# Optimization experiments

Hardware: AMD Instinct MI355X
Metric: run time of the kernel (lower is better)

## Reference

```python
import jax, jax.numpy as jnp
import numpy as np

SCALE = 0.08838834764831845  # 1/sqrt(128)


def setup_inputs() -> dict:
    key = jax.random.key(0)
    k1, k2, k3, k4 = jax.random.split(key, 4)
    B, Sq, H, D = 1, 2048, 32, 128
    Skv, K = 4096, 256
    return {
        "q": jax.random.normal(k1, (B, Sq, H, D), jnp.float32),
        "kv": jax.random.normal(k2, (B, Skv, 2, D), jnp.float32),  # stacked K,V (MQA)
        "attn_sink": jax.random.normal(k3, (H,), jnp.float32),
        "topk_idxs": jax.random.randint(k4, (B, Sq, K), 0, Skv),
    }


def reference(q, kv, attn_sink, topk_idxs):
    # q:        [B, Sq, H, D]
    # kv:       [B, Skv, 2, D]  (index 0 = keys, 1 = values; shared across heads)
    # topk_idxs:[B, Sq, K]      per-query selected KV positions
    # attn_sink:[H]             per-head sink logit added to the softmax denominator
    B = q.shape[0]
    # Gather selected KV per query: [B, Sq, K, 2, D]
    gathered = kv[jnp.arange(B)[:, None, None], topk_idxs]
    k = gathered[..., 0, :]  # [B, Sq, K, D]
    v = gathered[..., 1, :]  # [B, Sq, K, D]

    scores = jnp.einsum("bqhd,bqkd->bqhk", q, k) * SCALE  # [B, Sq, H, K]
    sink = attn_sink[None, None, :, None]                  # [1, 1, H, 1]

    # Numerically stable softmax over K selected tokens + sink logit.
    m = jnp.maximum(jnp.max(scores, axis=-1, keepdims=True), sink)
    e = jnp.exp(scores - m)
    denom = jnp.sum(e, axis=-1, keepdims=True) + jnp.exp(sink - m)
    probs = e / denom                                      # sink absorbs leftover mass

    out = jnp.einsum("bqhk,bqkd->bqhd", probs, v)          # [B, Sq, H, D]
    return out
```

## Files before the change

### kernel.cpp

```cpp
#include <hip/hip_runtime.h>
#include <hip/hip_bf16.h>

#define SQ 2048
#define NH 32
#define DH 128
#define NK 256
#define SCALE 0.08838834764831845f

typedef __attribute__((ext_vector_type(8))) __bf16 bf16x8;
typedef __attribute__((ext_vector_type(4))) float floatx4;
typedef __attribute__((ext_vector_type(4))) unsigned short ushort4_t;

#define QS_STRIDE 136
#define KS_STRIDE 136
#define VB_STRIDE 72
#define PB_STRIDE 264

#define OFF_KV   16896
#define OFF_TOPK 35328
#define OFF_SINK 36352
#define OFF_RED  36480
#define OFF_RED2 36992
#define SMEM_SZ  37504

__device__ __forceinline__ unsigned short f2bf(float x) {
  union { float f; unsigned int u; } v; v.f = x;
  unsigned int r = v.u + 0x7FFFu + ((v.u >> 16) & 1u);
  return (unsigned short)(r >> 16);
}

template <int CTRL>
__device__ __forceinline__ float dpp_rot(float x) {
  int i = __builtin_bit_cast(int, x);
  i = __builtin_amdgcn_mov_dpp(i, CTRL, 0xF, 0xF, true);
  return __builtin_bit_cast(float, i);
}
#define RED16_MAX(v) { v = fmaxf(v, dpp_rot<0x121>(v)); v = fmaxf(v, dpp_rot<0x122>(v)); \
                       v = fmaxf(v, dpp_rot<0x124>(v)); v = fmaxf(v, dpp_rot<0x128>(v)); }
#define RED16_SUM(v) { v += dpp_rot<0x121>(v); v += dpp_rot<0x122>(v); \
                       v += dpp_rot<0x124>(v); v += dpp_rot<0x128>(v); }

__global__ __launch_bounds__(256) void kv_to_bf16(const float* __restrict__ kv,
                                                  unsigned short* __restrict__ kvb) {
  int i = blockIdx.x * 256 + threadIdx.x;
  float4 f = ((const float4*)kv)[i];
  ushort4_t u = { f2bf(f.x), f2bf(f.y), f2bf(f.z), f2bf(f.w) };
  ((ushort4_t*)kvb)[i] = u;
}

__global__ __launch_bounds__(256, 4) void sparse_attn_kernel(
    const float* __restrict__ q, const unsigned short* __restrict__ kvb,
    const float* __restrict__ sink, const int* __restrict__ topk,
    float* __restrict__ out) {
  __shared__ __align__(16) char smem[SMEM_SZ];
  unsigned short* qs    = (unsigned short*)smem;
  unsigned short* pbuf  = (unsigned short*)smem;
  unsigned short* kvbuf = (unsigned short*)(smem + OFF_KV);
  int*   topk_s = (int*)(smem + OFF_TOPK);
  float* sink_s = (float*)(smem + OFF_SINK);
  float* red    = (float*)(smem + OFF_RED);
  float* red2   = (float*)(smem + OFF_RED2);

  const int tid = threadIdx.x;
  const int s = blockIdx.x;
  const int wave = tid >> 6;
  const int lane = tid & 63;
  const int quad = lane >> 4;
  const int l16 = lane & 15;

  topk_s[tid] = topk[(size_t)s * NK + tid];
  if (tid < 32) sink_s[tid] = sink[tid];
  {
    int r = tid >> 2, seg = tid & 3;
    int idx = topk[(size_t)s * NK + r];
    const unsigned short* kp = kvb + (size_t)idx * 256 + seg * 32;
    unsigned short* dst = &kvbuf[r * KS_STRIDE + seg * 32];
#pragma unroll
    for (int i = 0; i < 4; i++)
      *(uint4*)&dst[i * 8] = *(const uint4*)&kp[i * 8];
  }
  {
    const float* qp = q + (size_t)s * (NH * DH);
    int h = tid >> 3;
    int d0 = (tid & 7) * 16;
#pragma unroll
    for (int i = 0; i < 4; i++) {
      float4 f = *(const float4*)(qp + h * DH + d0 + i * 4);
      ushort4_t u = { f2bf(f.x * SCALE), f2bf(f.y * SCALE),
                      f2bf(f.z * SCALE), f2bf(f.w * SCALE) };
      *(ushort4_t*)&qs[h * QS_STRIDE + d0 + i * 4] = u;
    }
  }
  __syncthreads();

  bf16x8 afrag[2][4];
#pragma unroll
  for (int mt = 0; mt < 2; mt++)
#pragma unroll
    for (int ks = 0; ks < 4; ks++)
      afrag[mt][ks] =
          *(const bf16x8*)&qs[(mt * 16 + l16) * QS_STRIDE + ks * 32 + quad * 8];

  floatx4 sc[4][2];
#pragma unroll 1
  for (int c = 0; c < 4; c++) {
    floatx4 a0 = {0.f, 0.f, 0.f, 0.f};
    floatx4 a1 = {0.f, 0.f, 0.f, 0.f};
    const int nrow = wave * 16 + l16;
#pragma unroll
    for (int ks = 0; ks < 4; ks++) {
      bf16x8 b = *(const bf16x8*)&kvbuf[nrow * KS_STRIDE + ks * 32 + quad * 8];
      a0 = __builtin_amdgcn_mfma_f32_16x16x32_bf16(afrag[0][ks], b, a0, 0, 0, 0);
      a1 = __builtin_amdgcn_mfma_f32_16x16x32_bf16(afrag[1][ks], b, a1, 0, 0, 0);
    }
    sc[c][0] = a0;
    sc[c][1] = a1;
    __syncthreads();
    if (c < 3) {
      int r = tid >> 2, seg = tid & 3;
      int idx = topk_s[(c + 1) * 64 + r];
      const unsigned short* kp = kvb + (size_t)idx * 256 + seg * 32;
      unsigned short* dst = &kvbuf[r * KS_STRIDE + seg * 32];
#pragma unroll
      for (int i = 0; i < 4; i++)
        *(uint4*)&dst[i * 8] = *(const uint4*)&kp[i * 8];
      __syncthreads();
    }
  }

  {
    int rg = tid & 15, dg = tid >> 4;
    int r0 = rg * 4, d0 = dg * 8;
    int4 idx4 = *(const int4*)&topk_s[r0];
    uint4 ra = *(const uint4*)(kvb + (size_t)idx4.x * 256 + 128 + d0);
    uint4 rb = *(const uint4*)(kvb + (size_t)idx4.y * 256 + 128 + d0);
    uint4 rc = *(const uint4*)(kvb + (size_t)idx4.z * 256 + 128 + d0);
    uint4 rd = *(const uint4*)(kvb + (size_t)idx4.w * 256 + 128 + d0);
    const unsigned* pa = (const unsigned*)&ra;
    const unsigned* pb = (const unsigned*)&rb;
    const unsigned* pc = (const unsigned*)&rc;
    const unsigned* pd = (const unsigned*)&rd;
#pragma unroll
    for (int w = 0; w < 4; w++) {
      unsigned lo01 = __builtin_amdgcn_perm(pb[w], pa[w], 0x05040100u);
      unsigned lo23 = __builtin_amdgcn_perm(pd[w], pc[w], 0x05040100u);
      unsigned hi01 = __builtin_amdgcn_perm(pb[w], pa[w], 0x07060302u);
      unsigned hi23 = __builtin_amdgcn_perm(pd[w], pc[w], 0x07060302u);
      uint2 lo = { lo01, lo23 }, hi = { hi01, hi23 };
      *(uint2*)&kvbuf[(d0 + 2 * w) * VB_STRIDE + r0] = lo;
      *(uint2*)&kvbuf[(d0 + 2 * w + 1) * VB_STRIDE + r0] = hi;
    }
  }

  float mh[2][4];
#pragma unroll
  for (int mt = 0; mt < 2; mt++)
#pragma unroll
    for (int r = 0; r < 4; r++) {
      float v = fmaxf(fmaxf(sc[0][mt][r], sc[1][mt][r]),
                      fmaxf(sc[2][mt][r], sc[3][mt][r]));
      RED16_MAX(v);
      mh[mt][r] = v;
    }
  if (l16 == 0) {
#pragma unroll
    for (int mt = 0; mt < 2; mt++)
#pragma unroll
      for (int r = 0; r < 4; r++)
        red[wave * 32 + mt * 16 + quad * 4 + r] = mh[mt][r];
  }
  __syncthreads();
#pragma unroll
  for (int mt = 0; mt < 2; mt++)
#pragma unroll
    for (int r = 0; r < 4; r++) {
      int h = mt * 16 + quad * 4 + r;
      float v = sink_s[h];
#pragma unroll
      for (int w = 0; w < 4; w++) v = fmaxf(v, red[w * 32 + h]);
      mh[mt][r] = v;
    }
  float ps[2][4];
#pragma unroll
  for (int mt = 0; mt < 2; mt++)
#pragma unroll
    for (int r = 0; r < 4; r++) {
      float acc = 0.f;
#pragma unroll
      for (int c = 0; c < 4; c++) {
        float e = __expf(sc[c][mt][r] - mh[mt][r]);
        sc[c][mt][r] = e;
        acc += e;
      }
      RED16_SUM(acc);
      ps[mt][r] = acc;
    }
  if (l16 == 0) {
#pragma unroll
    for (int mt = 0; mt < 2; mt++)
#pragma unroll
      for (int r = 0; r < 4; r++)
        red2[wave * 32 + mt * 16 + quad * 4 + r] = ps[mt][r];
  }
  __syncthreads();
  float inv[2][4];
#pragma unroll
  for (int mt = 0; mt < 2; mt++)
#pragma unroll
    for (int r = 0; r < 4; r++) {
      int h = mt * 16 + quad * 4 + r;
      float dd = __expf(sink_s[h] - mh[mt][r]);
#pragma unroll
      for (int w = 0; w < 4; w++) dd += red2[w * 32 + h];
      inv[mt][r] = 1.0f / dd;
    }
#pragma unroll
  for (int c = 0; c < 4; c++)
#pragma unroll
    for (int mt = 0; mt < 2; mt++)
#pragma unroll
      for (int r = 0; r < 4; r++)
        pbuf[(mt * 16 + quad * 4 + r) * PB_STRIDE + c * 64 + wave * 16 + l16] =
            f2bf(sc[c][mt][r]);
  __syncthreads();

  floatx4 oacc[2][2];
#pragma unroll
  for (int mt = 0; mt < 2; mt++)
#pragma unroll
    for (int nt = 0; nt < 2; nt++)
      oacc[mt][nt] = (floatx4){0.f, 0.f, 0.f, 0.f};

#pragma unroll 1
  for (int c = 0; c < 4; c++) {
#pragma unroll
    for (int ks = 0; ks < 2; ks++) {
      int kof = c * 64 + ks * 32 + quad * 8;
      bf16x8 a0 = *(const bf16x8*)&pbuf[l16 * PB_STRIDE + kof];
      bf16x8 a1 = *(const bf16x8*)&pbuf[(16 + l16) * PB_STRIDE + kof];
      int kl = ks * 32 + quad * 8;
      bf16x8 b0 = *(const bf16x8*)&kvbuf[(wave * 32 + l16) * VB_STRIDE + kl];
      bf16x8 b1 = *(const bf16x8*)&kvbuf[(wave * 32 + 16 + l16) * VB_STRIDE + kl];
      oacc[0][0] = __builtin_amdgcn_mfma_f32_16x16x32_bf16(a0, b0, oacc[0][0], 0, 0, 0);
      oacc[0][1] = __builtin_amdgcn_mfma_f32_16x16x32_bf16(a0, b1, oacc[0][1], 0, 0, 0);
      oacc[1][0] = __builtin_amdgcn_mfma_f32_16x16x32_bf16(a1, b0, oacc[1][0], 0, 0, 0);
      oacc[1][1] = __builtin_amdgcn_mfma_f32_16x16x32_bf16(a1, b1, oacc[1][1], 0, 0, 0);
    }
    if (c < 3) {
      __syncthreads();
      int rg = tid & 15, dg = tid >> 4;
      int r0 = rg * 4, d0 = dg * 8;
      int4 idx4 = *(const int4*)&topk_s[(c + 1) * 64 + r0];
      uint4 ra = *(const uint4*)(kvb + (size_t)idx4.x * 256 + 128 + d0);
      uint4 rb = *(const uint4*)(kvb + (size_t)idx4.y * 256 + 128 + d0);
      uint4 rc = *(const uint4*)(kvb + (size_t)idx4.z * 256 + 128 + d0);
      uint4 rd = *(const uint4*)(kvb + (size_t)idx4.w * 256 + 128 + d0);
      const unsigned* pa = (const unsigned*)&ra;
      const unsigned* pb = (const unsigned*)&rb;
      const unsigned* pc = (const unsigned*)&rc;
      const unsigned* pd = (const unsigned*)&rd;
#pragma unroll
      for (int w = 0; w < 4; w++) {
        unsigned lo01 = __builtin_amdgcn_perm(pb[w], pa[w], 0x05040100u);
        unsigned lo23 = __builtin_amdgcn_perm(pd[w], pc[w], 0x05040100u);
        unsigned hi01 = __builtin_amdgcn_perm(pb[w], pa[w], 0x07060302u);
        unsigned hi23 = __builtin_amdgcn_perm(pd[w], pc[w], 0x07060302u);
        uint2 lo = { lo01, lo23 }, hi = { hi01, hi23 };
        *(uint2*)&kvbuf[(d0 + 2 * w) * VB_STRIDE + r0] = lo;
        *(uint2*)&kvbuf[(d0 + 2 * w + 1) * VB_STRIDE + r0] = hi;
      }
      __syncthreads();
    }
  }

  {
    float* op = out + (size_t)s * (NH * DH);
#pragma unroll
    for (int mt = 0; mt < 2; mt++)
#pragma unroll
      for (int nt = 0; nt < 2; nt++)
#pragma unroll
        for (int r4 = 0; r4 < 4; r4++) {
          int h = mt * 16 + quad * 4 + r4;
          int d = wave * 32 + nt * 16 + l16;
          op[h * DH + d] = oacc[mt][nt][r4] * inv[mt][r4];
        }
  }
}

extern "C" void kernel_launch(void* const* d_in, const int* in_sizes, int n_in,
                              void* d_out, int out_size, void* d_ws, size_t ws_size,
                              hipStream_t stream) {
  (void)in_sizes; (void)n_in; (void)out_size; (void)ws_size;
  const float* q    = (const float*)d_in[0];
  const float* kv   = (const float*)d_in[1];
  const float* sink = (const float*)d_in[2];
  const int*   topk = (const int*)d_in[3];
  float* out = (float*)d_out;
  unsigned short* kvb = (unsigned short*)d_ws;

  kv_to_bf16<<<dim3(1024), dim3(256), 0, stream>>>(kv, kvb);
  sparse_attn_kernel<<<dim3(SQ), dim3(256), 0, stream>>>(q, kvb, sink, topk, out);
}
```

Baseline: 117.5 us.

## Prefetch gathered K/V chunks into registers to overlap loads with MFMA

Restructures the K and V gather loops into a register-prefetch pipeline. The next chunk's global gather is issued before the current chunk's MFMA work, and the first V chunk is loaded during the softmax phase. This is meant to hide gather latency that was previously exposed between barriers. It also folds log2(e) into the Q scale and sink so exp2 can be used directly, and replaces manual bf16 rounding with packed conversion intrinsics, at the cost of higher register pressure.

```diff
diff --git a/kernel.cpp b/kernel.cpp
--- a/kernel.cpp
+++ b/kernel.cpp
@@ -6,10 +6,10 @@
 #define DH 128
 #define NK 256
 #define SCALE 0.08838834764831845f
+#define LOG2E 1.4426950408889634f
 
 typedef __attribute__((ext_vector_type(8))) __bf16 bf16x8;
 typedef __attribute__((ext_vector_type(4))) float floatx4;
-typedef __attribute__((ext_vector_type(4))) unsigned short ushort4_t;
 
 #define QS_STRIDE 136
 #define KS_STRIDE 136
@@ -23,10 +23,18 @@
 #define OFF_RED2 36992
 #define SMEM_SZ  37504
 
-__device__ __forceinline__ unsigned short f2bf(float x) {
-  union { float f; unsigned int u; } v; v.f = x;
-  unsigned int r = v.u + 0x7FFFu + ((v.u >> 16) & 1u);
-  return (unsigned short)(r >> 16);
+__device__ __forceinline__ unsigned pk_bf16(float a, float b) {
+  union { __hip_bfloat162 h2; unsigned u; } c;
+  c.h2 = __float22bfloat162_rn(make_float2(a, b));
+  return c.u;
+}
+
+__device__ __forceinline__ float fast_exp2(float x) {
+#if __has_builtin(__builtin_amdgcn_exp2f)
+  return __builtin_amdgcn_exp2f(x);
+#else
+  return exp2f(x);
+#endif
 }
 
 template <int CTRL>
@@ -44,8 +52,93 @@
                                                   unsigned short* __restrict__ kvb) {
   int i = blockIdx.x * 256 + threadIdx.x;
   float4 f = ((const float4*)kv)[i];
-  ushort4_t u = { f2bf(f.x), f2bf(f.y), f2bf(f.z), f2bf(f.w) };
-  ((ushort4_t*)kvb)[i] = u;
+  uint2 o = { pk_bf16(f.x, f.y), pk_bf16(f.z, f.w) };
+  ((uint2*)kvb)[i] = o;
+}
+
+struct KR { uint4 v[4]; };
+struct VR { uint4 a, b, c, d; };
+
+__device__ __forceinline__ KR k_load(const unsigned short* __restrict__ kvb,
+                                     const int* __restrict__ tks, int c, int tid) {
+  int r = tid >> 2, seg = tid & 3;
+  int idx = tks[c * 64 + r];
+  const uint4* p = (const uint4*)(kvb + (size_t)idx * 256 + seg * 32);
+  KR k;
+#pragma unroll
+  for (int i = 0; i < 4; i++) k.v[i] = p[i];
+  return k;
+}
+
+__device__ __forceinline__ void k_write(unsigned short* kvbuf, const KR& k, int tid) {
+  int r = tid >> 2, seg = tid & 3;
+  uint4* d = (uint4*)&kvbuf[r * KS_STRIDE + seg * 32];
+#pragma unroll
+  for (int i = 0; i < 4; i++) d[i] = k.v[i];
+}
+
+__device__ __forceinline__ VR v_load(const unsigned short* __restrict__ kvb,
+                                     const int* tks, int c, int tid) {
+  int rg = tid & 15, dg = tid >> 4;
+  int r0 = rg * 4, d0 = dg * 8;
+  int4 i4 = *(const int4*)&tks[c * 64 + r0];
+  VR v;
+  v.a = *(const uint4*)(kvb + (size_t)i4.x * 256 + 128 + d0);
+  v.b = *(const uint4*)(kvb + (size_t)i4.y * 256 + 128 + d0);
+  v.c = *(const uint4*)(kvb + (size_t)i4.z * 256 + 128 + d0);
+  v.d = *(const uint4*)(kvb + (size_t)i4.w * 256 + 128 + d0);
+  return v;
+}
+
+__device__ __forceinline__ void v_write(unsigned short* kvbuf, const VR& v, int tid) {
+  int rg = tid & 15, dg = tid >> 4;
+  int r0 = rg * 4, d0 = dg * 8;
+  const unsigned* pa = (const unsigned*)&v.a;
+  const unsigned* pb = (const unsigned*)&v.b;
+  const unsigned* pc = (const unsigned*)&v.c;
+  const unsigned* pd = (const unsigned*)&v.d;
+#pragma unroll
+  for (int w = 0; w < 4; w++) {
+    unsigned lo01 = __builtin_amdgcn_perm(pb[w], pa[w], 0x05040100u);
+    unsigned lo23 = __builtin_amdgcn_perm(pd[w], pc[w], 0x05040100u);
+    unsigned hi01 = __builtin_amdgcn_perm(pb[w], pa[w], 0x07060302u);
+    unsigned hi23 = __builtin_amdgcn_perm(pd[w], pc[w], 0x07060302u);
+    uint2 lo = { lo01, lo23 }, hi = { hi01, hi23 };
+    *(uint2*)&kvbuf[(d0 + 2 * w) * VB_STRIDE + r0] = lo;
+    *(uint2*)&kvbuf[(d0 + 2 * w + 1) * VB_STRIDE + r0] = hi;
+  }
+}
+
+__device__ __forceinline__ void gemm1(const unsigned short* kvbuf,
+                                      const bf16x8 af[2][4], int nrow, int quad,
+                                      floatx4& a0, floatx4& a1) {
+  a0 = (floatx4){0.f, 0.f, 0.f, 0.f};
+  a1 = (floatx4){0.f, 0.f, 0.f, 0.f};
+#pragma unroll
+  for (int ks = 0; ks < 4; ks++) {
+    bf16x8 b = *(const bf16x8*)&kvbuf[nrow * KS_STRIDE + ks * 32 + quad * 8];
+    a0 = __builtin_amdgcn_mfma_f32_16x16x32_bf16(af[0][ks], b, a0, 0, 0, 0);
+    a1 = __builtin_amdgcn_mfma_f32_16x16x32_bf16(af[1][ks], b, a1, 0, 0, 0);
+  }
+}
+
+__device__ __forceinline__ void pv_chunk(const unsigned short* pbuf,
+                                         const unsigned short* kvbuf, int c,
+                                         int wave, int quad, int l16,
+                                         floatx4 oacc[2][2]) {
+#pragma unroll
+  for (int ks = 0; ks < 2; ks++) {
+    int kof = c * 64 + ks * 32 + quad * 8;
+    bf16x8 a0 = *(const bf16x8*)&pbuf[l16 * PB_STRIDE + kof];
+    bf16x8 a1 = *(const bf16x8*)&pbuf[(16 + l16) * PB_STRIDE + kof];
+    int kl = ks * 32 + quad * 8;
+    bf16x8 b0 = *(const bf16x8*)&kvbuf[(wave * 32 + l16) * VB_STRIDE + kl];
+    bf16x8 b1 = *(const bf16x8*)&kvbuf[(wave * 32 + 16 + l16) * VB_STRIDE + kl];
+    oacc[0][0] = __builtin_amdgcn_mfma_f32_16x16x32_bf16(a0, b0, oacc[0][0], 0, 0, 0);
+    oacc[0][1] = __builtin_amdgcn_mfma_f32_16x16x32_bf16(a0, b1, oacc[0][1], 0, 0, 0);
+    oacc[1][0] = __builtin_amdgcn_mfma_f32_16x16x32_bf16(a1, b0, oacc[1][0], 0, 0, 0);
+    oacc[1][1] = __builtin_amdgcn_mfma_f32_16x16x32_bf16(a1, b1, oacc[1][1], 0, 0, 0);
+  }
 }
 
 __global__ __launch_bounds__(256, 4) void sparse_attn_kernel(
@@ -67,30 +160,32 @@
   const int lane = tid & 63;
   const int quad = lane >> 4;
   const int l16 = lane & 15;
-
-  topk_s[tid] = topk[(size_t)s * NK + tid];
-  if (tid < 32) sink_s[tid] = sink[tid];
+  const int* tkg = topk + (size_t)s * NK;
+
+  topk_s[tid] = tkg[tid];
+  if (tid < 32) sink_s[tid] = sink[tid] * LOG2E;
   {
     int r = tid >> 2, seg = tid & 3;
-    int idx = topk[(size_t)s * NK + r];
-    const unsigned short* kp = kvb + (size_t)idx * 256 + seg * 32;
-    unsigned short* dst = &kvbuf[r * KS_STRIDE + seg * 32];
-#pragma unroll
-    for (int i = 0; i < 4; i++)
-      *(uint4*)&dst[i * 8] = *(const uint4*)&kp[i * 8];
+    int idx = tkg[r];
+    const uint4* p = (const uint4*)(kvb + (size_t)idx * 256 + seg * 32);
+    uint4* d = (uint4*)&kvbuf[r * KS_STRIDE + seg * 32];
+#pragma unroll
+    for (int i = 0; i < 4; i++) d[i] = p[i];
   }
   {
+    const float QSC = SCALE * LOG2E;
     const float* qp = q + (size_t)s * (NH * DH);
-    int h = tid >> 3;
-    int d0 = (tid & 7) * 16;
-#pragma unroll
-    for (int i = 0; i < 4; i++) {
-      float4 f = *(const float4*)(qp + h * DH + d0 + i * 4);
-      ushort4_t u = { f2bf(f.x * SCALE), f2bf(f.y * SCALE),
-                      f2bf(f.z * SCALE), f2bf(f.w * SCALE) };
-      *(ushort4_t*)&qs[h * QS_STRIDE + d0 + i * 4] = u;
-    }
-  }
+    int h = tid >> 3, d0 = (tid & 7) * 16;
+    const float4* src = (const float4*)(qp + h * DH + d0);
+    float4 f0 = src[0], f1 = src[1], f2 = src[2], f3 = src[3];
+    uint4 o0 = { pk_bf16(f0.x * QSC, f0.y * QSC), pk_bf16(f0.z * QSC, f0.w * QSC),
+                 pk_bf16(f1.x * QSC, f1.y * QSC), pk_bf16(f1.z * QSC, f1.w * QSC) };
+    uint4 o1 = { pk_bf16(f2.x * QSC, f2.y * QSC), pk_bf16(f2.z * QSC, f2.w * QSC),
+                 pk_bf16(f3.x * QSC, f3.y * QSC), pk_bf16(f3.z * QSC, f3.w * QSC) };
+    *(uint4*)&qs[h * QS_STRIDE + d0] = o0;
+    *(uint4*)&qs[h * QS_STRIDE + d0 + 8] = o1;
+  }
+  KR k1 = k_load(kvb, tkg, 1, tid);
   __syncthreads();
 
   bf16x8 afrag[2][4];
@@ -101,56 +196,31 @@
       afrag[mt][ks] =
           *(const bf16x8*)&qs[(mt * 16 + l16) * QS_STRIDE + ks * 32 + quad * 8];
 
+  const int nrow = wave * 16 + l16;
+
   floatx4 sc[4][2];
-#pragma unroll 1
-  for (int c = 0; c < 4; c++) {
-    floatx4 a0 = {0.f, 0.f, 0.f, 0.f};
-    floatx4 a1 = {0.f, 0.f, 0.f, 0.f};
-    const int nrow = wave * 16 + l16;
-#pragma unroll
-    for (int ks = 0; ks < 4; ks++) {
-      bf16x8 b = *(const bf16x8*)&kvbuf[nrow * KS_STRIDE + ks * 32 + quad * 8];
-      a0 = __builtin_amdgcn_mfma_f32_16x16x32_bf16(afrag[0][ks], b, a0, 0, 0, 0);
-      a1 = __builtin_amdgcn_mfma_f32_16x16x32_bf16(afrag[1][ks], b, a1, 0, 0, 0);
-    }
-    sc[c][0] = a0;
-    sc[c][1] = a1;
-    __syncthreads();
-    if (c < 3) {
-      int r = tid >> 2, seg = tid & 3;
-      int idx = topk_s[(c + 1) * 64 + r];
-      const unsigned short* kp = kvb + (size_t)idx * 256 + seg * 32;
-      unsigned short* dst = &kvbuf[r * KS_STRIDE + seg * 32];
-#pragma unroll
-      for (int i = 0; i < 4; i++)
-        *(uint4*)&dst[i * 8] = *(const uint4*)&kp[i * 8];
-      __syncthreads();
-    }
-  }
-
-  {
-    int rg = tid & 15, dg = tid >> 4;
-    int r0 = rg * 4, d0 = dg * 8;
-    int4 idx4 = *(const int4*)&topk_s[r0];
-    uint4 ra = *(const uint4*)(kvb + (size_t)idx4.x * 256 + 128 + d0);
-    uint4 rb = *(const uint4*)(kvb + (size_t)idx4.y * 256 + 128 + d0);
-    uint4 rc = *(const uint4*)(kvb + (size_t)idx4.z * 256 + 128 + d0);
-    uint4 rd = *(const uint4*)(kvb + (size_t)idx4.w * 256 + 128 + d0);
-    const unsigned* pa = (const unsigned*)&ra;
-    const unsigned* pb = (const unsigned*)&rb;
-    const unsigned* pc = (const unsigned*)&rc;
-    const unsigned* pd = (const unsigned*)&rd;
-#pragma unroll
-    for (int w = 0; w < 4; w++) {
-      unsigned lo01 = __builtin_amdgcn_perm(pb[w], pa[w], 0x05040100u);
-      unsigned lo23 = __builtin_amdgcn_perm(pd[w], pc[w], 0x05040100u);
-      unsigned hi01 = __builtin_amdgcn_perm(pb[w], pa[w], 0x07060302u);
-      unsigned hi23 = __builtin_amdgcn_perm(pd[w], pc[w], 0x07060302u);
-      uint2 lo = { lo01, lo23 }, hi = { hi01, hi23 };
-      *(uint2*)&kvbuf[(d0 + 2 * w) * VB_STRIDE + r0] = lo;
-      *(uint2*)&kvbuf[(d0 + 2 * w + 1) * VB_STRIDE + r0] = hi;
-    }
-  }
+  gemm1(kvbuf, afrag, nrow, quad, sc[0][0], sc[0][1]);
+  __syncthreads();
+  k_write(kvbuf, k1, tid);
+  KR k2 = k_load(kvb, topk_s, 2, tid);
+  __syncthreads();
+
+  gemm1(kvbuf, afrag, nrow, quad, sc[1][0], sc[1][1]);
+  __syncthreads();
+  k_write(kvbuf, k2, tid);
+  KR k3 = k_load(kvb, topk_s, 3, tid);
+  __syncthreads();
+
+  gemm1(kvbuf, afrag, nrow, quad, sc[2][0], sc[2][1]);
+  __syncthreads();
+  k_write(kvbuf, k3, tid);
+  VR v0 = v_load(kvb, topk_s, 0, tid);
+  __syncthreads();
+
+  gemm1(kvbuf, afrag, nrow, quad, sc[3][0], sc[3][1]);
+  __syncthreads();
+  v_write(kvbuf, v0, tid);
+  VR v1 = v_load(kvb, topk_s, 1, tid);
 
   float mh[2][4];
 #pragma unroll
@@ -188,7 +258,7 @@
       float acc = 0.f;
 #pragma unroll
       for (int c = 0; c < 4; c++) {
-        float e = __expf(sc[c][mt][r] - mh[mt][r]);
+        float e = fast_exp2(sc[c][mt][r] - mh[mt][r]);
         sc[c][mt][r] = e;
         acc += e;
       }
@@ -209,7 +279,7 @@
 #pragma unroll
     for (int r = 0; r < 4; r++) {
       int h = mt * 16 + quad * 4 + r;
-      float dd = __expf(sink_s[h] - mh[mt][r]);
+      float dd = fast_exp2(sink_s[h] - mh[mt][r]);
 #pragma unroll
       for (int w = 0; w < 4; w++) dd += red2[w * 32 + h];
       inv[mt][r] = 1.0f / dd;
@@ -217,11 +287,16 @@
 #pragma unroll
   for (int c = 0; c < 4; c++)
 #pragma unroll
-    for (int mt = 0; mt < 2; mt++)
-#pragma unroll
-      for (int r = 0; r < 4; r++)
-        pbuf[(mt * 16 + quad * 4 + r) * PB_STRIDE + c * 64 + wave * 16 + l16] =
-            f2bf(sc[c][mt][r]);
+    for (int mt = 0; mt < 2; mt++) {
+      int col = c * 64 + wave * 16 + l16;
+      unsigned short* pb = &pbuf[(mt * 16 + quad * 4) * PB_STRIDE + col];
+      unsigned p01 = pk_bf16(sc[c][mt][0], sc[c][mt][1]);
+      unsigned p23 = pk_bf16(sc[c][mt][2], sc[c][mt][3]);
+      pb[0] = (unsigned short)p01;
+      pb[PB_STRIDE] = (unsigned short)(p01 >> 16);
+      pb[2 * PB_STRIDE] = (unsigned short)p23;
+      pb[3 * PB_STRIDE] = (unsigned short)(p23 >> 16);
+    }
   __syncthreads();
 
   floatx4 oacc[2][2];
@@ -231,47 +306,24 @@
     for (int nt = 0; nt < 2; nt++)
       oacc[mt][nt] = (floatx4){0.f, 0.f, 0.f, 0.f};
 
-#pragma unroll 1
-  for (int c = 0; c < 4; c++) {
-#pragma unroll
-    for (int ks = 0; ks < 2; ks++) {
-      int kof = c * 64 + ks * 32 + quad * 8;
-      bf16x8 a0 = *(const bf16x8*)&pbuf[l16 * PB_STRIDE + kof];
-      bf16x8 a1 = *(const bf16x8*)&pbuf[(16 + l16) * PB_STRIDE + kof];
-      int kl = ks * 32 + quad * 8;
-      bf16x8 b0 = *(const bf16x8*)&kvbuf[(wave * 32 + l16) * VB_STRIDE + kl];
-      bf16x8 b1 = *(const bf16x8*)&kvbuf[(wave * 32 + 16 + l16) * VB_STRIDE + kl];
-      oacc[0][0] = __builtin_amdgcn_mfma_f32_16x16x32_bf16(a0, b0, oacc[0][0], 0, 0, 0);
-      oacc[0][1] = __builtin_amdgcn_mfma_f32_16x16x32_bf16(a0, b1, oacc[0][1], 0, 0, 0);
-      oacc[1][0] = __builtin_amdgcn_mfma_f32_16x16x32_bf16(a1, b0, oacc[1][0], 0, 0, 0);
-      oacc[1][1] = __builtin_amdgcn_mfma_f32_16x16x32_bf16(a1, b1, oacc[1][1], 0, 0, 0);
-    }
-    if (c < 3) {
-      __syncthreads();
-      int rg = tid & 15, dg = tid >> 4;
-      int r0 = rg * 4, d0 = dg * 8;
-      int4 idx4 = *(const int4*)&topk_s[(c + 1) * 64 + r0];
-      uint4 ra = *(const uint4*)(kvb + (size_t)idx4.x * 256 + 128 + d0);
-      uint4 rb = *(const uint4*)(kvb + (size_t)idx4.y * 256 + 128 + d0);
-      uint4 rc = *(const uint4*)(kvb + (size_t)idx4.z * 256 + 128 + d0);
-      uint4 rd = *(const uint4*)(kvb + (size_t)idx4.w * 256 + 128 + d0);
-      const unsigned* pa = (const unsigned*)&ra;
-      const unsigned* pb = (const unsigned*)&rb;
-      const unsigned* pc = (const unsigned*)&rc;
-      const unsigned* pd = (const unsigned*)&rd;
-#pragma unroll
-      for (int w = 0; w < 4; w++) {
-        unsigned lo01 = __builtin_amdgcn_perm(pb[w], pa[w], 0x05040100u);
-        unsigned lo23 = __builtin_amdgcn_perm(pd[w], pc[w], 0x05040100u);
-        unsigned hi01 = __builtin_amdgcn_perm(pb[w], pa[w], 0x07060302u);
-        unsigned hi23 = __builtin_amdgcn_perm(pd[w], pc[w], 0x07060302u);
-        uint2 lo = { lo01, lo23 }, hi = { hi01, hi23 };
-        *(uint2*)&kvbuf[(d0 + 2 * w) * VB_STRIDE + r0] = lo;
-        *(uint2*)&kvbuf[(d0 + 2 * w + 1) * VB_STRIDE + r0] = hi;
-      }
-      __syncthreads();
-    }
-  }
+  pv_chunk(pbuf, kvbuf, 0, wave, quad, l16, oacc);
+  __syncthreads();
+  v_write(kvbuf, v1, tid);
+  VR v2 = v_load(kvb, topk_s, 2, tid);
+  __syncthreads();
+
+  pv_chunk(pbuf, kvbuf, 1, wave, quad, l16, oacc);
+  __syncthreads();
+  v_write(kvbuf, v2, tid);
+  VR v3 = v_load(kvb, topk_s, 3, tid);
+  __syncthreads();
+
+  pv_chunk(pbuf, kvbuf, 2, wave, quad, l16, oacc);
+  __syncthreads();
+  v_write(kvbuf, v3, tid);
+  __syncthreads();
+
+  pv_chunk(pbuf, kvbuf, 3, wave, quad, l16, oacc);
 
   {
     float* op = out + (size_t)s * (NH * DH);
```

Result: faster. 113.4 us (-3.5%).
